# Performance work log

Measured on AMD Instinct MI355X. Metric: run time of the kernel, lower is better.

The kernel has to match this reference:

```python
import jax, jax.numpy as jnp
import numpy as np

B, T, F, U = 256, 1024, 64, 128  # batch, history_size, model_input_num, GRU units


def gru(x_seq, W, Uk, b, return_sequences):
    """Keras GRU (reset_after=True, recurrent_activation=sigmoid, activation=relu).
    x_seq: [B,T,F_in]; W: [F_in,3U]; Uk: [U,3U]; b: [2,3U] (input bias, recurrent bias).
    """
    b_i, b_r = b[0], b[1]
    xw = jnp.einsum('bti,iu->btu', x_seq, W) + b_i  # precompute input projection [B,T,3U]

    def step(h, xw_t):
        rec = h @ Uk + b_r                          # [B,3U]
        xz, xr, xh = jnp.split(xw_t, 3, axis=-1)
        rz, rr, rh = jnp.split(rec, 3, axis=-1)
        z = jax.nn.sigmoid(xz + rz)
        r = jax.nn.sigmoid(xr + rr)
        hh = jax.nn.relu(xh + r * rh)
        h_new = z * h + (1.0 - z) * hh
        return h_new, h_new

    h0 = jnp.zeros((x_seq.shape[0], Uk.shape[0]), dtype=x_seq.dtype)
    hT, hs = jax.lax.scan(step, h0, jnp.swapaxes(xw, 0, 1))  # scan over time
    if return_sequences:
        return jnp.swapaxes(hs, 0, 1), hT  # [B,T,U], [B,U]
    return hT, hT


def setup_inputs() -> dict:
    key = jax.random.key(0)
    ks = jax.random.split(key, 7)
    s_in1 = 1.0 / np.sqrt(F)
    s_rec = 1.0 / np.sqrt(U)
    return {
        'input_data': jax.random.normal(ks[0], (B, T, F), dtype=jnp.float32),
        'W1': jax.random.normal(ks[1], (F, 3 * U), dtype=jnp.float32) * s_in1,
        'U1': jax.random.normal(ks[2], (U, 3 * U), dtype=jnp.float32) * s_rec,
        'b1': jnp.zeros((2, 3 * U), dtype=jnp.float32),
        'W2': jax.random.normal(ks[3], (U, 3 * U), dtype=jnp.float32) * s_rec,
        'U2': jax.random.normal(ks[4], (U, 3 * U), dtype=jnp.float32) * s_rec,
        'b2': jnp.zeros((2, 3 * U), dtype=jnp.float32),
    }


def reference(input_data, W1, U1, b1, W2, U2, b2):
    seq1, state1 = gru(input_data, W1, U1, b1, return_sequences=True)
    x, state2 = gru(seq1, W2, U2, b2, return_sequences=False)
    return (x, state1, state2)
```

## Files before the change

kernel.cpp:

```cpp
#include <hip/hip_runtime.h>


#define TT 1024
#define FF 64
#define G3 384
#define NB 16
#define CHUNK 64
#define NCH (TT / CHUNK)
#define FLAG_BYTES 1024
#define H1F_BYTES ((size_t)NB * TT * 4096)
#define PIPE_WS (FLAG_BYTES + H1F_BYTES)

typedef __attribute__((ext_vector_type(8))) __bf16 bf16x8;
typedef __attribute__((ext_vector_type(4))) float f32x4;

#define MFMA(a, b, c) __builtin_amdgcn_mfma_f32_16x16x32_bf16((a), (b), (c), 0, 0, 0)

__device__ __forceinline__ float sigf(float x) {
    return __builtin_amdgcn_rcpf(1.0f + __expf(-x));
}

__device__ __forceinline__ void wait_flag(const unsigned int* f) {
    while (__hip_atomic_load(f, __ATOMIC_ACQUIRE, __HIP_MEMORY_SCOPE_AGENT) == 0u)
        __builtin_amdgcn_s_sleep(1);
}

__global__ __launch_bounds__(512)
__attribute__((amdgpu_waves_per_eu(2, 2)))
void gru_pipe2(
    const float* __restrict__ x,  const float* __restrict__ W1,
    const float* __restrict__ U1, const float* __restrict__ b1,
    const float* __restrict__ W2, const float* __restrict__ U2,
    const float* __restrict__ b2, unsigned char* __restrict__ ws,
    float* __restrict__ out)
{
    const int tid  = threadIdx.x;
    const int wave = tid >> 6;
    const int lane = tid & 63;
    const int quad = lane >> 4;
    const int lc   = lane & 15;
    const int rb   = blockIdx.x & 15;
    const int row0 = rb * 16;
    const int u    = wave * 16 + lc;

    unsigned int* flags = (unsigned int*)ws + rb * NCH;
    unsigned char* h1f  = ws + FLAG_BYTES + (size_t)rb * TT * 4096;

    __shared__ __align__(16) __bf16 hs[2][16][136];
    for (int i = tid; i < 2 * 16 * 136; i += 512)
        ((__bf16*)hs)[i] = (__bf16)0.f;

    const f32x4 zeroq = {0.f, 0.f, 0.f, 0.f};

    if (blockIdx.x < NB) {
        bf16x8 U1B[3][4], W1B[3][2];
#pragma unroll
        for (int g = 0; g < 3; g++) {
#pragma unroll
            for (int kt = 0; kt < 4; kt++) {
                bf16x8 a;
#pragma unroll
                for (int j = 0; j < 8; j++)
                    a[j] = (__bf16)U1[(kt * 32 + quad * 8 + j) * G3 + g * 128 + u];
                U1B[g][kt] = a;
            }
#pragma unroll
            for (int kt = 0; kt < 2; kt++) {
                bf16x8 a;
#pragma unroll
                for (int j = 0; j < 8; j++)
                    a[j] = (__bf16)W1[(kt * 32 + quad * 8 + j) * G3 + g * 128 + u];
                W1B[kt == 0 ? g : g][kt] = a;
            }
        }
        const float c1z  = b1[u] + b1[G3 + u];
        const float c1r  = b1[128 + u] + b1[G3 + 128 + u];
        const float b1ih = b1[256 + u];
        const float b1rh = b1[G3 + 256 + u];
        const f32x4 c1zq  = {c1z, c1z, c1z, c1z};
        const f32x4 c1rq  = {c1r, c1r, c1r, c1r};
        const f32x4 b1ihq = {b1ih, b1ih, b1ih, b1ih};
        const f32x4 b1rhq = {b1rh, b1rh, b1rh, b1rh};

        const float* xrow = x + (size_t)(row0 + lc) * (TT * FF) + quad * 8;
        f32x4 xp0 = *(const f32x4*)(xrow);
        f32x4 xp1 = *(const f32x4*)(xrow + 4);
        f32x4 xp2 = *(const f32x4*)(xrow + 32);
        f32x4 xp3 = *(const f32x4*)(xrow + 36);

        float h1c[4] = {0, 0, 0, 0};
        __syncthreads();

#define PSTEP(T, PAR)                                                          \
    {                                                                          \
        bf16x8 A1[4];                                                          \
        _Pragma("unroll") for (int kt = 0; kt < 4; kt++)                       \
            A1[kt] = *(const bf16x8*)&hs[PAR ^ 1][lc][kt * 32 + quad * 8];     \
        bf16x8 xa0, xa1;                                                       \
        _Pragma("unroll") for (int j = 0; j < 4; j++) {                        \
            xa0[j] = (__bf16)xp0[j]; xa0[j + 4] = (__bf16)xp1[j];              \
            xa1[j] = (__bf16)xp2[j]; xa1[j + 4] = (__bf16)xp3[j];              \
        }                                                                      \
        if ((T) + 1 < TT) {                                                    \
            const float* px = xrow + (size_t)((T) + 1) * FF;                   \
            xp0 = *(const f32x4*)px;                                           \
            xp1 = *(const f32x4*)(px + 4);                                     \
            xp2 = *(const f32x4*)(px + 32);                                    \
            xp3 = *(const f32x4*)(px + 36);                                    \
        }                                                                      \
                    \
        f32x4 z1a = MFMA(xa0, W1B[0][0], c1zq);                                \
        f32x4 r1a = MFMA(xa0, W1B[1][0], c1rq);                                \
        f32x4 xh1 = MFMA(xa0, W1B[2][0], b1ihq);                               \
        z1a = MFMA(xa1, W1B[0][1], z1a);                                       \
        r1a = MFMA(xa1, W1B[1][1], r1a);                                       \
        xh1 = MFMA(xa1, W1B[2][1], xh1);                                       \
                           \
        f32x4 z1b = MFMA(A1[0], U1B[0][0], zeroq);                             \
        f32x4 r1b = MFMA(A1[0], U1B[1][0], zeroq);                             \
        f32x4 rh1 = MFMA(A1[0], U1B[2][0], b1rhq);                             \
        _Pragma("unroll") for (int kt = 1; kt < 4; kt++) {                     \
            z1b = MFMA(A1[kt], U1B[0][kt], z1b);                               \
            r1b = MFMA(A1[kt], U1B[1][kt], r1b);                               \
            rh1 = MFMA(A1[kt], U1B[2][kt], rh1);                               \
        }                                                                      \
        if ((T) > 0 && wave == 0) {        \
            _Pragma("unroll") for (int kt = 0; kt < 4; kt++)                   \
                *(bf16x8*)(h1f + ((size_t)((T) - 1) * 4 + kt) * 1024           \
                           + lane * 16) = A1[kt];                              \
        }                                                                      \
        f32x4 z1 = z1a + z1b;                                                  \
        f32x4 r1 = r1a + r1b;                                                  \
        _Pragma("unroll") for (int i = 0; i < 4; i++) {                        \
            float zf = sigf(z1[i]);                                            \
            float rf = sigf(r1[i]);                                            \
            float hh = fmaxf(xh1[i] + rf * rh1[i], 0.f);                       \
            h1c[i] = fmaf(zf, h1c[i] - hh, hh);                                \
            hs[PAR][quad * 4 + i][u] = (__bf16)h1c[i];                         \
        }                                                                      \
        if (wave == 0 && (T) > 0 && (((T) & 63) == 0)) {                       \
            __threadfence();                                                   \
            if (lane == 0)                                                     \
                __hip_atomic_store(flags + ((T) >> 6) - 1, 1u,                 \
                                   __ATOMIC_RELEASE,                           \
                                   __HIP_MEMORY_SCOPE_AGENT);                  \
        }                                                                      \
        asm volatile("s_waitcnt lgkmcnt(0)\n\ts_barrier" ::: "memory");        \
    }

        for (int t = 0; t < TT; t += 2) {
            PSTEP(t, 0)
            PSTEP(t + 1, 1)
        }
#undef PSTEP

        if (wave == 0) {
#pragma unroll
            for (int kt = 0; kt < 4; kt++) {
                bf16x8 a = *(const bf16x8*)&hs[1][lc][kt * 32 + quad * 8];
                *(bf16x8*)(h1f + ((size_t)(TT - 1) * 4 + kt) * 1024
                           + lane * 16) = a;
            }
            __threadfence();
            if (lane == 0)
                __hip_atomic_store(flags + NCH - 1, 1u, __ATOMIC_RELEASE,
                                   __HIP_MEMORY_SCOPE_AGENT);
        }
#pragma unroll
        for (int i = 0; i < 4; i++) {
            int r = row0 + quad * 4 + i;
            out[32768 + (size_t)r * 128 + u] = h1c[i];
        }
    } else {
        bf16x8 W2B[3][4], U2B[3][4];
#pragma unroll
        for (int g = 0; g < 3; g++)
#pragma unroll
            for (int kt = 0; kt < 4; kt++) {
                bf16x8 b, c;
#pragma unroll
                for (int j = 0; j < 8; j++) {
                    int k = (kt * 32 + quad * 8 + j) * G3 + g * 128 + u;
                    b[j] = (__bf16)W2[k];
                    c[j] = (__bf16)U2[k];
                }
                W2B[g][kt] = b;
                U2B[g][kt] = c;
            }
        const float c2z  = b2[u] + b2[G3 + u];
        const float c2r  = b2[128 + u] + b2[G3 + 128 + u];
        const float b2ih = b2[256 + u];
        const float b2rh = b2[G3 + 256 + u];
        const f32x4 c2zq  = {c2z, c2z, c2z, c2z};
        const f32x4 c2rq  = {c2r, c2r, c2r, c2r};
        const f32x4 b2ihq = {b2ih, b2ih, b2ih, b2ih};
        const f32x4 b2rhq = {b2rh, b2rh, b2rh, b2rh};

        float h2c[4] = {0, 0, 0, 0};
        bf16x8 hAa0, hAa1, hAa2, hAa3, hAb0, hAb1, hAb2, hAb3;
        __syncthreads();

#define CSTEP(T, PAR, C0, C1, C2, C3)                                          \
    {                                                                          \
        bf16x8 A2[4];                                                          \
        _Pragma("unroll") for (int kt = 0; kt < 4; kt++)                       \
            A2[kt] = *(const bf16x8*)&hs[PAR ^ 1][lc][kt * 32 + quad * 8];     \
                    \
        f32x4 z2a = MFMA(C0, W2B[0][0], c2zq);                                 \
        f32x4 r2a = MFMA(C0, W2B[1][0], c2rq);                                 \
        f32x4 xh2 = MFMA(C0, W2B[2][0], b2ihq);                                \
        z2a = MFMA(C1, W2B[0][1], z2a);                                        \
        r2a = MFMA(C1, W2B[1][1], r2a);                                        \
        xh2 = MFMA(C1, W2B[2][1], xh2);                                        \
        z2a = MFMA(C2, W2B[0][2], z2a);                                        \
        r2a = MFMA(C2, W2B[1][2], r2a);                                        \
        xh2 = MFMA(C2, W2B[2][2], xh2);                                        \
        z2a = MFMA(C3, W2B[0][3], z2a);                                        \
        r2a = MFMA(C3, W2B[1][3], r2a);                                        \
        xh2 = MFMA(C3, W2B[2][3], xh2);                                        \
        if ((T) + 2 < tend) {      \
            const unsigned char* sp =                                          \
                h1f + (size_t)((T) + 2) * 4096 + lane * 16;                    \
            C0 = *(const bf16x8*)(sp);                                         \
            C1 = *(const bf16x8*)(sp + 1024);                                  \
            C2 = *(const bf16x8*)(sp + 2048);                                  \
            C3 = *(const bf16x8*)(sp + 3072);                                  \
        }                                                                      \
                           \
        f32x4 z2b = MFMA(A2[0], U2B[0][0], zeroq);                             \
        f32x4 r2b = MFMA(A2[0], U2B[1][0], zeroq);                             \
        f32x4 rh2 = MFMA(A2[0], U2B[2][0], b2rhq);                             \
        _Pragma("unroll") for (int kt = 1; kt < 4; kt++) {                     \
            z2b = MFMA(A2[kt], U2B[0][kt], z2b);                               \
            r2b = MFMA(A2[kt], U2B[1][kt], r2b);                               \
            rh2 = MFMA(A2[kt], U2B[2][kt], rh2);                               \
        }                                                                      \
        f32x4 z2 = z2a + z2b;                                                  \
        f32x4 r2 = r2a + r2b;                                                  \
        _Pragma("unroll") for (int i = 0; i < 4; i++) {                        \
            float zf = sigf(z2[i]);                                            \
            float rf = sigf(r2[i]);                                            \
            float hh = fmaxf(xh2[i] + rf * rh2[i], 0.f);                       \
            h2c[i] = fmaf(zf, h2c[i] - hh, hh);                                \
            hs[PAR][quad * 4 + i][u] = (__bf16)h2c[i];                         \
        }                                                                      \
        asm volatile("s_waitcnt lgkmcnt(0)\n\ts_barrier" ::: "memory");        \
    }

        for (int c = 0; c < NCH; c++) {
            wait_flag(flags + c);
            const int t0   = c * CHUNK;
            const int tend = t0 + CHUNK;
            {
                const unsigned char* sp = h1f + (size_t)t0 * 4096 + lane * 16;
                hAa0 = *(const bf16x8*)(sp);
                hAa1 = *(const bf16x8*)(sp + 1024);
                hAa2 = *(const bf16x8*)(sp + 2048);
                hAa3 = *(const bf16x8*)(sp + 3072);
                const unsigned char* sq = sp + 4096;
                hAb0 = *(const bf16x8*)(sq);
                hAb1 = *(const bf16x8*)(sq + 1024);
                hAb2 = *(const bf16x8*)(sq + 2048);
                hAb3 = *(const bf16x8*)(sq + 3072);
            }
            for (int t = t0; t < tend; t += 2) {
                CSTEP(t, 0, hAa0, hAa1, hAa2, hAa3)
                CSTEP(t + 1, 1, hAb0, hAb1, hAb2, hAb3)
            }
        }
#undef CSTEP

#pragma unroll
        for (int i = 0; i < 4; i++) {
            int r = row0 + quad * 4 + i;
            out[(size_t)r * 128 + u]         = h2c[i];
            out[65536 + (size_t)r * 128 + u] = h2c[i];
        }
    }
}

__global__ __launch_bounds__(512)
__attribute__((amdgpu_waves_per_eu(2, 2)))
void gru_mono(
    const float* __restrict__ x,  const float* __restrict__ W1,
    const float* __restrict__ U1, const float* __restrict__ b1,
    const float* __restrict__ W2, const float* __restrict__ U2,
    const float* __restrict__ b2, float* __restrict__ out)
{
    const int tid  = threadIdx.x;
    const int wave = tid >> 6;
    const int lane = tid & 63;
    const int quad = lane >> 4;
    const int lc   = lane & 15;
    const int row0 = blockIdx.x * 16;
    const int u    = wave * 16 + lc;

    __shared__ __align__(16) __bf16 h1s[2][16][136];
    __shared__ __align__(16) __bf16 h2s[2][16][136];
    for (int i = tid; i < 2 * 16 * 136; i += 512) {
        ((__bf16*)h1s)[i] = (__bf16)0.f;
        ((__bf16*)h2s)[i] = (__bf16)0.f;
    }

    bf16x8 U1B[3][4], W2B[3][4], U2B[3][4], W1B[3][2];
#pragma unroll
    for (int g = 0; g < 3; g++) {
#pragma unroll
        for (int kt = 0; kt < 4; kt++) {
            bf16x8 a, b, c;
#pragma unroll
            for (int j = 0; j < 8; j++) {
                int k = (kt * 32 + quad * 8 + j) * G3 + g * 128 + u;
                a[j] = (__bf16)U1[k];
                b[j] = (__bf16)W2[k];
                c[j] = (__bf16)U2[k];
            }
            U1B[g][kt] = a; W2B[g][kt] = b; U2B[g][kt] = c;
        }
#pragma unroll
        for (int kt = 0; kt < 2; kt++) {
            bf16x8 a;
#pragma unroll
            for (int j = 0; j < 8; j++)
                a[j] = (__bf16)W1[(kt * 32 + quad * 8 + j) * G3 + g * 128 + u];
            W1B[g][kt] = a;
        }
    }

    const float c1z  = b1[u] + b1[G3 + u];
    const float c1r  = b1[128 + u] + b1[G3 + 128 + u];
    const float b1ih = b1[256 + u];
    const float b1rh = b1[G3 + 256 + u];
    const float c2z  = b2[u] + b2[G3 + u];
    const float c2r  = b2[128 + u] + b2[G3 + 128 + u];
    const float b2ih = b2[256 + u];
    const float b2rh = b2[G3 + 256 + u];
    const f32x4 c1zq  = {c1z, c1z, c1z, c1z};
    const f32x4 c1rq  = {c1r, c1r, c1r, c1r};
    const f32x4 b1ihq = {b1ih, b1ih, b1ih, b1ih};
    const f32x4 b1rhq = {b1rh, b1rh, b1rh, b1rh};
    const f32x4 c2zq  = {c2z, c2z, c2z, c2z};
    const f32x4 c2rq  = {c2r, c2r, c2r, c2r};
    const f32x4 b2ihq = {b2ih, b2ih, b2ih, b2ih};
    const f32x4 b2rhq = {b2rh, b2rh, b2rh, b2rh};

    const float* xrow = x + (size_t)(row0 + lc) * (TT * FF) + quad * 8;
    float h1c[4] = {0, 0, 0, 0};
    float h2c[4] = {0, 0, 0, 0};
    __syncthreads();

#define MSTEP(T, PAR)                                                          \
    {                                                                          \
        bf16x8 A1[4];                                                          \
        _Pragma("unroll") for (int kt = 0; kt < 4; kt++)                       \
            A1[kt] = *(const bf16x8*)&h1s[PAR ^ 1][lc][kt * 32 + quad * 8];    \
        const float* px = xrow + (size_t)(T) * FF;                             \
        f32x4 u0 = *(const f32x4*)px;                                          \
        f32x4 u1 = *(const f32x4*)(px + 4);                                    \
        f32x4 u2 = *(const f32x4*)(px + 32);                                   \
        f32x4 u3 = *(const f32x4*)(px + 36);                                   \
        bf16x8 xa0, xa1;                                                       \
        _Pragma("unroll") for (int j = 0; j < 4; j++) {                        \
            xa0[j] = (__bf16)u0[j]; xa0[j + 4] = (__bf16)u1[j];                \
            xa1[j] = (__bf16)u2[j]; xa1[j + 4] = (__bf16)u3[j];                \
        }                                                                      \
        f32x4 z1  = MFMA(xa0, W1B[0][0], c1zq);                                \
        z1        = MFMA(xa1, W1B[0][1], z1);                                  \
        f32x4 r1  = MFMA(xa0, W1B[1][0], c1rq);                                \
        r1        = MFMA(xa1, W1B[1][1], r1);                                  \
        f32x4 xh1 = MFMA(xa0, W1B[2][0], b1ihq);                               \
        xh1       = MFMA(xa1, W1B[2][1], xh1);                                 \
        f32x4 rh1 = MFMA(A1[0], U1B[2][0], b1rhq);                             \
        z1        = MFMA(A1[0], U1B[0][0], z1);                                \
        r1        = MFMA(A1[0], U1B[1][0], r1);                                \
        _Pragma("unroll") for (int kt = 1; kt < 4; kt++) {                     \
            z1  = MFMA(A1[kt], U1B[0][kt], z1);                                \
            r1  = MFMA(A1[kt], U1B[1][kt], r1);                                \
            rh1 = MFMA(A1[kt], U1B[2][kt], rh1);                               \
        }                                                                      \
        _Pragma("unroll") for (int i = 0; i < 4; i++) {                        \
            float zf = sigf(z1[i]);                                            \
            float rf = sigf(r1[i]);                                            \
            float hh = fmaxf(xh1[i] + rf * rh1[i], 0.f);                       \
            h1c[i] = fmaf(zf, h1c[i] - hh, hh);                                \
            h1s[PAR][quad * 4 + i][u] = (__bf16)h1c[i];                        \
        }                                                                      \
        f32x4 z2  = MFMA(A1[0], W2B[0][0], c2zq);                              \
        f32x4 r2  = MFMA(A1[0], W2B[1][0], c2rq);                              \
        f32x4 xh2 = MFMA(A1[0], W2B[2][0], b2ihq);                             \
        _Pragma("unroll") for (int kt = 1; kt < 4; kt++) {                     \
            z2  = MFMA(A1[kt], W2B[0][kt], z2);                                \
            r2  = MFMA(A1[kt], W2B[1][kt], r2);                                \
            xh2 = MFMA(A1[kt], W2B[2][kt], xh2);                               \
        }                                                                      \
        f32x4 rh2;                                                             \
        {                                                                      \
            bf16x8 A2 = *(const bf16x8*)&h2s[PAR][lc][quad * 8];               \
            rh2 = MFMA(A2, U2B[2][0], b2rhq);                                  \
            z2  = MFMA(A2, U2B[0][0], z2);                                     \
            r2  = MFMA(A2, U2B[1][0], r2);                                     \
        }                                                                      \
        _Pragma("unroll") for (int kt = 1; kt < 4; kt++) {                     \
            bf16x8 A2 = *(const bf16x8*)&h2s[PAR][lc][kt * 32 + quad * 8];     \
            z2  = MFMA(A2, U2B[0][kt], z2);                                    \
            r2  = MFMA(A2, U2B[1][kt], r2);                                    \
            rh2 = MFMA(A2, U2B[2][kt], rh2);                                   \
        }                                                                      \
        if ((T) > 0) {                                                         \
            _Pragma("unroll") for (int i = 0; i < 4; i++) {                    \
                float zf = sigf(z2[i]);                                        \
                float rf = sigf(r2[i]);                                        \
                float hh = fmaxf(xh2[i] + rf * rh2[i], 0.f);                   \
                h2c[i] = fmaf(zf, h2c[i] - hh, hh);                            \
            }                                                                  \
        }                                                                      \
        _Pragma("unroll") for (int i = 0; i < 4; i++)                          \
            h2s[PAR ^ 1][quad * 4 + i][u] = (__bf16)h2c[i];                    \
        asm volatile("s_waitcnt lgkmcnt(0)\n\ts_barrier" ::: "memory");        \
    }

    for (int t = 0; t < TT; t += 2) {
        MSTEP(t, 0)
        MSTEP(t + 1, 1)
    }
#undef MSTEP

    {
        f32x4 z2 = c2zq, r2 = c2rq, xh2 = b2ihq, rh2 = b2rhq;
#pragma unroll
        for (int kt = 0; kt < 4; kt++) {
            bf16x8 a1 = *(const bf16x8*)&h1s[1][lc][kt * 32 + quad * 8];
            bf16x8 a2 = *(const bf16x8*)&h2s[0][lc][kt * 32 + quad * 8];
            z2  = MFMA(a1, W2B[0][kt], z2);
            r2  = MFMA(a1, W2B[1][kt], r2);
            xh2 = MFMA(a1, W2B[2][kt], xh2);
            z2  = MFMA(a2, U2B[0][kt], z2);
            r2  = MFMA(a2, U2B[1][kt], r2);
            rh2 = MFMA(a2, U2B[2][kt], rh2);
        }
#pragma unroll
        for (int i = 0; i < 4; i++) {
            float zf = sigf(z2[i]);
            float rf = sigf(r2[i]);
            float hh = fmaxf(xh2[i] + rf * rh2[i], 0.f);
            h2c[i] = fmaf(zf, h2c[i] - hh, hh);
        }
    }

#pragma unroll
    for (int i = 0; i < 4; i++) {
        int r = row0 + quad * 4 + i;
        out[(size_t)r * 128 + u]         = h2c[i];
        out[32768 + (size_t)r * 128 + u] = h1c[i];
        out[65536 + (size_t)r * 128 + u] = h2c[i];
    }
}

extern "C" void kernel_launch(void* const* d_in, const int* in_sizes, int n_in,
                              void* d_out, int out_size, void* d_ws, size_t ws_size,
                              hipStream_t stream) {
    const float* x  = (const float*)d_in[0];
    const float* W1 = (const float*)d_in[1];
    const float* U1 = (const float*)d_in[2];
    const float* b1 = (const float*)d_in[3];
    const float* W2 = (const float*)d_in[4];
    const float* U2 = (const float*)d_in[5];
    const float* b2 = (const float*)d_in[6];
    float* out = (float*)d_out;

    if (ws_size >= PIPE_WS) {
        hipMemsetAsync(d_ws, 0, FLAG_BYTES, stream);
        gru_pipe2<<<dim3(2 * NB), dim3(512), 0, stream>>>(
            x, W1, U1, b1, W2, U2, b2, (unsigned char*)d_ws, out);
    } else {
        gru_mono<<<dim3(NB), dim3(512), 0, stream>>>(
            x, W1, U1, b1, W2, U2, b2, out);
    }
}
```

Baseline: 1.080 ms.

## Split MFMA accumulation chains, shrink pipeline chunk, and pad LDS hidden-state rows

Splits the z and r gate MFMA accumulation chains in both GRU layers into two independent accumulators that are summed at the end, shortening the dependent MFMA latency chain on the serial recurrence path. Halves the layer-1 to layer-2 handoff chunk size from 64 to 32 steps, so layer 2 can start sooner at the cost of more flag stores and waits. Pads the LDS hidden-state row from 136 to 140 bf16 to change the bank mapping. The extra accumulators add register pressure and a few vector adds per step.

```diff
diff --git a/kernel.cpp b/kernel.cpp
--- a/kernel.cpp
+++ b/kernel.cpp
@@ -5,9 +5,9 @@
 #define FF 64
 #define G3 384
 #define NB 16
-#define CHUNK 64
+#define CHUNK 32
 #define NCH (TT / CHUNK)
-#define FLAG_BYTES 1024
+#define FLAG_BYTES ((size_t)NB * NCH * 4)
 #define H1F_BYTES ((size_t)NB * TT * 4096)
 #define PIPE_WS (FLAG_BYTES + H1F_BYTES)
 
@@ -46,8 +46,8 @@
     unsigned int* flags = (unsigned int*)ws + rb * NCH;
     unsigned char* h1f  = ws + FLAG_BYTES + (size_t)rb * TT * 4096;
 
-    __shared__ __align__(16) __bf16 hs[2][16][136];
-    for (int i = tid; i < 2 * 16 * 136; i += 512)
+    __shared__ __align__(16) __bf16 hs[2][16][140];
+    for (int i = tid; i < 2 * 16 * 140; i += 512)
         ((__bf16*)hs)[i] = (__bf16)0.f;
 
     const f32x4 zeroq = {0.f, 0.f, 0.f, 0.f};
@@ -70,7 +70,7 @@
 #pragma unroll
                 for (int j = 0; j < 8; j++)
                     a[j] = (__bf16)W1[(kt * 32 + quad * 8 + j) * G3 + g * 128 + u];
-                W1B[kt == 0 ? g : g][kt] = a;
+                W1B[g][kt] = a;
             }
         }
         const float c1z  = b1[u] + b1[G3 + u];
@@ -115,22 +115,26 @@
         z1a = MFMA(xa1, W1B[0][1], z1a);                                       \
         r1a = MFMA(xa1, W1B[1][1], r1a);                                       \
         xh1 = MFMA(xa1, W1B[2][1], xh1);                                       \
-                           \
+                                     \
         f32x4 z1b = MFMA(A1[0], U1B[0][0], zeroq);                             \
         f32x4 r1b = MFMA(A1[0], U1B[1][0], zeroq);                             \
         f32x4 rh1 = MFMA(A1[0], U1B[2][0], b1rhq);                             \
-        _Pragma("unroll") for (int kt = 1; kt < 4; kt++) {                     \
-            z1b = MFMA(A1[kt], U1B[0][kt], z1b);                               \
-            r1b = MFMA(A1[kt], U1B[1][kt], r1b);                               \
-            rh1 = MFMA(A1[kt], U1B[2][kt], rh1);                               \
-        }                                                                      \
+        f32x4 z1d = MFMA(A1[1], U1B[0][1], zeroq);                             \
+        f32x4 r1d = MFMA(A1[1], U1B[1][1], zeroq);                             \
+        rh1 = MFMA(A1[1], U1B[2][1], rh1);                                     \
+        z1b = MFMA(A1[2], U1B[0][2], z1b);                                     \
+        r1b = MFMA(A1[2], U1B[1][2], r1b);                                     \
+        rh1 = MFMA(A1[2], U1B[2][2], rh1);                                     \
+        z1d = MFMA(A1[3], U1B[0][3], z1d);                                     \
+        r1d = MFMA(A1[3], U1B[1][3], r1d);                                     \
+        rh1 = MFMA(A1[3], U1B[2][3], rh1);                                     \
         if ((T) > 0 && wave == 0) {        \
             _Pragma("unroll") for (int kt = 0; kt < 4; kt++)                   \
                 *(bf16x8*)(h1f + ((size_t)((T) - 1) * 4 + kt) * 1024           \
                            + lane * 16) = A1[kt];                              \
         }                                                                      \
-        f32x4 z1 = z1a + z1b;                                                  \
-        f32x4 r1 = r1a + r1b;                                                  \
+        f32x4 z1 = z1a + (z1b + z1d);                                          \
+        f32x4 r1 = r1a + (r1b + r1d);                                          \
         _Pragma("unroll") for (int i = 0; i < 4; i++) {                        \
             float zf = sigf(z1[i]);                                            \
             float rf = sigf(r1[i]);                                            \
@@ -138,10 +142,10 @@
             h1c[i] = fmaf(zf, h1c[i] - hh, hh);                                \
             hs[PAR][quad * 4 + i][u] = (__bf16)h1c[i];                         \
         }                                                                      \
-        if (wave == 0 && (T) > 0 && (((T) & 63) == 0)) {                       \
+        if (wave == 0 && (T) > 0 && (((T) & (CHUNK - 1)) == 0)) {              \
             __threadfence();                                                   \
             if (lane == 0)                                                     \
-                __hip_atomic_store(flags + ((T) >> 6) - 1, 1u,                 \
+                __hip_atomic_store(flags + ((T) / CHUNK) - 1, 1u,              \
                                    __ATOMIC_RELEASE,                           \
                                    __HIP_MEMORY_SCOPE_AGENT);                  \
         }                                                                      \
@@ -209,14 +213,14 @@
         f32x4 z2a = MFMA(C0, W2B[0][0], c2zq);                                 \
         f32x4 r2a = MFMA(C0, W2B[1][0], c2rq);                                 \
         f32x4 xh2 = MFMA(C0, W2B[2][0], b2ihq);                                \
-        z2a = MFMA(C1, W2B[0][1], z2a);                                        \
-        r2a = MFMA(C1, W2B[1][1], r2a);                                        \
+        f32x4 z2c = MFMA(C1, W2B[0][1], zeroq);                                \
+        f32x4 r2c = MFMA(C1, W2B[1][1], zeroq);                                \
         xh2 = MFMA(C1, W2B[2][1], xh2);                                        \
         z2a = MFMA(C2, W2B[0][2], z2a);                                        \
         r2a = MFMA(C2, W2B[1][2], r2a);                                        \
         xh2 = MFMA(C2, W2B[2][2], xh2);                                        \
-        z2a = MFMA(C3, W2B[0][3], z2a);                                        \
-        r2a = MFMA(C3, W2B[1][3], r2a);                                        \
+        z2c = MFMA(C3, W2B[0][3], z2c);                                        \
+        r2c = MFMA(C3, W2B[1][3], r2c);                                        \
         xh2 = MFMA(C3, W2B[2][3], xh2);                                        \
         if ((T) + 2 < tend) {      \
             const unsigned char* sp =                                          \
@@ -226,17 +230,21 @@
             C2 = *(const bf16x8*)(sp + 2048);                                  \
             C3 = *(const bf16x8*)(sp + 3072);                                  \
         }                                                                      \
-                           \
+                                     \
         f32x4 z2b = MFMA(A2[0], U2B[0][0], zeroq);                             \
         f32x4 r2b = MFMA(A2[0], U2B[1][0], zeroq);                             \
         f32x4 rh2 = MFMA(A2[0], U2B[2][0], b2rhq);                             \
-        _Pragma("unroll") for (int kt = 1; kt < 4; kt++) {                     \
-            z2b = MFMA(A2[kt], U2B[0][kt], z2b);                               \
-            r2b = MFMA(A2[kt], U2B[1][kt], r2b);                               \
-            rh2 = MFMA(A2[kt], U2B[2][kt], rh2);                               \
-        }                                                                      \
-        f32x4 z2 = z2a + z2b;                                                  \
-        f32x4 r2 = r2a + r2b;                                                  \
+        f32x4 z2d = MFMA(A2[1], U2B[0][1], zeroq);                             \
+        f32x4 r2d = MFMA(A2[1], U2B[1][1], zeroq);                             \
+        rh2 = MFMA(A2[1], U2B[2][1], rh2);                                     \
+        z2b = MFMA(A2[2], U2B[0][2], z2b);                                     \
+        r2b = MFMA(A2[2], U2B[1][2], r2b);                                     \
+        rh2 = MFMA(A2[2], U2B[2][2], rh2);                                     \
+        z2d = MFMA(A2[3], U2B[0][3], z2d);                                     \
+        r2d = MFMA(A2[3], U2B[1][3], r2d);                                     \
+        rh2 = MFMA(A2[3], U2B[2][3], rh2);                                     \
+        f32x4 z2 = (z2a + z2c) + (z2b + z2d);                                  \
+        f32x4 r2 = (r2a + r2c) + (r2b + r2d);                                  \
         _Pragma("unroll") for (int i = 0; i < 4; i++) {                        \
             float zf = sigf(z2[i]);                                            \
             float rf = sigf(r2[i]);                                            \
```

Measured after the change: 1.069 ms. About the same (-1.1%).
